# Kernel tuning notes

Measured on AMD Instinct MI355X. Metric: run time of the kernel, lower is better.

The kernel has to match this reference:

```python
import jax, jax.numpy as jnp
import numpy as np

# Module config (matches init_kwargs)
DIM = 256
NUM_HEADS = 8
AREA = 4
B, C, H, W = 8, DIM, 64, 64
HEAD_DIM = DIM // NUM_HEADS

# Each Conv in the source is Conv2d(bias=False) + BatchNorm2d + Identity (activation=False).
# In eval mode BN is a per-channel affine, so we represent each Conv as (weight, scale, bias).

def setup_inputs() -> dict:
    key = jax.random.key(0)
    ks = jax.random.split(key, 13)
    def w(k, shape, s=0.05):
        return jax.random.normal(k, shape, jnp.float32) * s
    def bn_scale(k, n):
        return 1.0 + 0.02 * jax.random.normal(k, (n,), jnp.float32)
    x = jax.random.normal(ks[0], (B, C, H, W), jnp.float32)
    return {
        "x": x,
        "w_qk": w(ks[1], (2 * C, C)),        # 1x1 conv: [out,in]
        "s_qk": bn_scale(ks[2], 2 * C),
        "b_qk": w(ks[3], (2 * C,), 0.01),
        "w_v": w(ks[4], (C, C)),
        "s_v": bn_scale(ks[5], C),
        "b_v": w(ks[6], (C,), 0.01),
        "w_pe": w(ks[7], (C, 1, 5, 5)),       # depthwise 5x5, groups=C
        "s_pe": bn_scale(ks[8], C),
        "b_pe": w(ks[9], (C,), 0.01),
        "w_proj": w(ks[10], (C, C)),
        "s_proj": bn_scale(ks[11], C),
        "b_proj": w(ks[12], (C,), 0.01),
    }


def _affine(y, s, b):
    # per-channel BN-eval affine on NCHW
    return y * s[None, :, None, None] + b[None, :, None, None]


def _conv1x1(x, w, s, b):
    return _affine(jnp.einsum('bchw,oc->bohw', x, w), s, b)


def reference(x, w_qk, s_qk, b_qk, w_v, s_v, b_v, w_pe, s_pe, b_pe, w_proj, s_proj, b_proj):
    N = H * W
    Na = N // AREA
    Ba = B * AREA

    qk = _conv1x1(x, w_qk, s_qk, b_qk)                    # [B, 2C, H, W]
    v4 = _conv1x1(x, w_v, s_v, b_v)                       # [B, C, H, W]
    pp = _affine(
        jax.lax.conv_general_dilated(
            v4, w_pe, (1, 1), 'SAME', feature_group_count=C,
            dimension_numbers=('NCHW', 'OIHW', 'NCHW')),
        s_pe, b_pe)                                        # [B, C, H, W]

    # flatten(2).transpose(1,2) then area split along N
    qk = qk.reshape(B, 2 * C, N).transpose(0, 2, 1).reshape(Ba, Na, 2 * C)
    v = v4.reshape(B, C, N).transpose(0, 2, 1).reshape(Ba, Na, C)

    q = qk[..., :C].reshape(Ba, Na, NUM_HEADS, HEAD_DIM)
    k = qk[..., C:].reshape(Ba, Na, NUM_HEADS, HEAD_DIM)
    vh = v.reshape(Ba, Na, NUM_HEADS, HEAD_DIM)

    scale = jnp.asarray(HEAD_DIM, jnp.float32) ** -0.5
    attn = jnp.einsum('bqhd,bkhd->bhqk', q, k) * scale     # [Ba, h, Na, Na]
    attn = jax.nn.softmax(attn, axis=-1)                   # max-stable softmax over keys
    o = jnp.einsum('bhqk,bkhd->bqhd', attn, vh)            # [Ba, Na, h, d]
    o = o.reshape(Ba, Na, C).reshape(B, N, C)
    o = o.reshape(B, H, W, C).transpose(0, 3, 1, 2)        # [B, C, H, W]

    return _conv1x1(o + pp, w_proj, s_proj, b_proj)
```

## Files before the change

### kernel.cpp

```cpp
#include <hip/hip_runtime.h>
#include <math.h>


#define NN 4096
#define NA 1024

typedef unsigned short us;
typedef __attribute__((ext_vector_type(4))) unsigned short us4;
typedef __attribute__((ext_vector_type(8))) unsigned short us8;
typedef __attribute__((ext_vector_type(8))) short bf16x8;
typedef __attribute__((ext_vector_type(4))) float f32x4;

#define QS (0.17677669529663687f * 1.4426950408889634f)

__device__ __forceinline__ us f2b(float f) {
    unsigned u = __builtin_bit_cast(unsigned, f);
    u += 0x7fffu + ((u >> 16) & 1u);
    return (us)(u >> 16);
}
__device__ __forceinline__ float b2f(us h) {
    unsigned u = ((unsigned)h) << 16;
    return __builtin_bit_cast(float, u);
}
__device__ __forceinline__ unsigned pack2(float lo, float hi) {
    return (unsigned)f2b(lo) | ((unsigned)f2b(hi) << 16);
}
__device__ __forceinline__ unsigned cvtpk_bf16(float lo, float hi) {
    unsigned r;
    asm("v_cvt_pk_bf16_f32 %0, %1, %2" : "=v"(r) : "v"(lo), "v"(hi));
    return r;
}
__device__ __forceinline__ float fexp2(float x) {
    float r;
    asm("v_exp_f32 %0, %1" : "=v"(r) : "v"(x));
    return r;
}

__device__ __forceinline__ size_t wswz(int ch, int k) {
    return ((size_t)((ch >> 4) * 8 + (k >> 5))) * 512 + ((((k >> 3) & 3) * 16 + (ch & 15))) * 8 + (k & 7);
}

__global__ __launch_bounds__(256) void prep_kernel(
    const float* __restrict__ w_qk, const float* __restrict__ s_qk, const float* __restrict__ b_qk,
    const float* __restrict__ w_v,  const float* __restrict__ s_v,
    const float* __restrict__ w_proj, const float* __restrict__ s_proj,
    us* __restrict__ wqkh, us* __restrict__ wvh, us* __restrict__ wprojh,
    float* __restrict__ bqkp)
{
    int idx = blockIdx.x * 256 + threadIdx.x;
    if (idx < 131072) {
        int o = idx >> 8, k = idx & 255;
        float sc = s_qk[o] * (o < 256 ? QS : 1.0f);
        wqkh[wswz(o, k)] = f2b(w_qk[idx] * sc);
    } else if (idx < 196608) {
        int j = idx - 131072; int o = j >> 8, k = j & 255;
        wvh[wswz(o, k)] = f2b(w_v[j] * s_v[o]);
    } else {
        int j = idx - 196608; int o = j >> 8, k = j & 255;
        wprojh[wswz(o, k)] = f2b(w_proj[j] * s_proj[o]);
    }
    if (idx < 512) bqkp[idx] = b_qk[idx] * (idx < 256 ? QS : 1.0f);
}

__global__ __launch_bounds__(256) void qkv_kernel(
    const float* __restrict__ x,
    const us* __restrict__ wqkh, const float* __restrict__ bqkp,
    const us* __restrict__ wvh,  const float* __restrict__ b_v,
    us* __restrict__ qt, us* __restrict__ vbuf)
{
    const int n0 = blockIdx.x * 64;
    const int b  = blockIdx.y;
    const int tid = threadIdx.x;
    const int w = tid >> 6, lane = tid & 63, c = lane & 15, g = lane >> 4;

    __shared__ __align__(16) us Xs[64][264];

    const float* Xb = x + (size_t)b * 256 * NN;
    #pragma unroll
    for (int i = 0; i < 16; i++) {
        int t = tid + i * 256;
        int cp = t >> 5, pp = t & 31;
        const float* r0 = Xb + (size_t)(2 * cp) * NN + n0 + 2 * pp;
        float2 a0 = *(const float2*)r0;
        float2 a1 = *(const float2*)(r0 + NN);
        *(unsigned*)&Xs[2 * pp][2 * cp]     = pack2(a0.x, a1.x);
        *(unsigned*)&Xs[2 * pp + 1][2 * cp] = pack2(a0.y, a1.y);
    }
    __syncthreads();

    for (int grp = 0; grp < 3; grp++) {
        f32x4 acc[4][4] = {};
        for (int kc = 0; kc < 256; kc += 32) {
            bf16x8 Xf[4];
            #pragma unroll
            for (int j = 0; j < 4; j++)
                Xf[j] = *(const bf16x8*)&Xs[j * 16 + c][kc + g * 8];
            #pragma unroll
            for (int cgi = 0; cgi < 4; cgi++) {
                int chbase = (grp < 2 ? (grp * 4 + cgi) * 64 : cgi * 64);
                const us* Wp = (grp < 2 ? wqkh : wvh) +
                    ((size_t)(((chbase >> 4) + w) * 8 + (kc >> 5))) * 512 + lane * 8;
                bf16x8 Wf = *(const bf16x8*)Wp;
                if (grp < 2) {
                    #pragma unroll
                    for (int j = 0; j < 4; j++)
                        acc[cgi][j] = __builtin_amdgcn_mfma_f32_16x16x32_bf16(Xf[j], Wf, acc[cgi][j], 0, 0, 0);
                } else {
                    #pragma unroll
                    for (int j = 0; j < 4; j++)
                        acc[cgi][j] = __builtin_amdgcn_mfma_f32_16x16x32_bf16(Wf, Xf[j], acc[cgi][j], 0, 0, 0);
                }
            }
        }
        if (grp < 2) {
            #pragma unroll
            for (int cgi = 0; cgi < 4; cgi++) {
                int ch = (grp * 4 + cgi) * 64 + w * 16 + c;
                float bb = bqkp[ch];
                #pragma unroll
                for (int j = 0; j < 4; j++)
                    #pragma unroll
                    for (int r = 0; r < 4; r++)
                        qt[((size_t)b * 4096 + n0 + j * 16 + g * 4 + r) * 512 + ch] =
                            f2b(acc[cgi][j][r] + bb);
            }
        } else {
            #pragma unroll
            for (int cgi = 0; cgi < 4; cgi++)
                #pragma unroll
                for (int r = 0; r < 4; r++) {
                    int ch = cgi * 64 + w * 16 + g * 4 + r;
                    float bb = b_v[ch];
                    #pragma unroll
                    for (int j = 0; j < 4; j++)
                        vbuf[((size_t)b * 256 + ch) * NN + n0 + j * 16 + c] =
                            f2b(acc[cgi][j][r] + bb);
                }
        }
    }
}

__global__ __launch_bounds__(256) void pe_conv_kernel(
    const us* __restrict__ vbuf,
    const float* __restrict__ w_pe, const float* __restrict__ s_pe, const float* __restrict__ b_pe,
    float* __restrict__ opp)
{
    const int c = blockIdx.x, b = blockIdx.y;
    const int tid = threadIdx.x;
    const us* vp = vbuf + ((size_t)b * 256 + c) * NN;
    __shared__ float plane[4096];
    __shared__ float wloc[25];
    #pragma unroll
    for (int i = 0; i < 4; i++) {
        int idx = tid + i * 256;
        us4 v = *(const us4*)&vp[idx * 4];
        float4 f;
        f.x = b2f(v[0]); f.y = b2f(v[1]); f.z = b2f(v[2]); f.w = b2f(v[3]);
        *(float4*)&plane[idx * 4] = f;
    }
    if (tid < 25) wloc[tid] = w_pe[c * 25 + tid];
    __syncthreads();

    const float s = s_pe[c], bb = b_pe[c];
    float* op = opp + ((size_t)b * 256 + c) * NN;
    for (int i = 0; i < 16; i++) {
        int pix = tid + i * 256;
        int ph = pix >> 6, pw = pix & 63;
        float acc = 0.f;
        #pragma unroll
        for (int dy = -2; dy <= 2; dy++) {
            int hy = ph + dy;
            if (hy < 0 || hy > 63) continue;
            #pragma unroll
            for (int dx = -2; dx <= 2; dx++) {
                int wx = pw + dx;
                if (wx < 0 || wx > 63) continue;
                acc += plane[hy * 64 + wx] * wloc[(dy + 2) * 5 + (dx + 2)];
            }
        }
        op[pix] = acc * s + bb;
    }
}

__global__ __launch_bounds__(256) void attn_kernel(
    const us* __restrict__ qt, const us* __restrict__ vbuf, float* __restrict__ opp)
{
    const int qtb = blockIdx.x;
    const int h   = blockIdx.y;
    const int ba  = blockIdx.z;
    const int b = ba >> 2, a = ba & 3;
    const int tid = threadIdx.x;
    const int w = tid >> 6, lane = tid & 63, c = lane & 15, g = lane >> 4;
    const int q0 = qtb * 128;

    __shared__ __align__(16) us Qt[128][40];
    __shared__ __align__(16) us Kt[2][64][40];
    __shared__ __align__(16) us Vs[2][2048];
    __shared__ __align__(16) us Ps[128][72];

    const int krow = tid >> 2, kseg = tid & 3;
    const int vrow = tid >> 3, vseg = tid & 7;
    const int vbyte = vrow * 128 + ((vseg ^ (vrow & 7)) << 4);

    const us* Kg = qt + ((size_t)b * 4096 + a * NA) * 512 + 256 + h * 32;
    const us* Vg = vbuf + ((size_t)b * 256 + h * 32) * NN + a * NA;

    #pragma unroll
    for (int i = 0; i < 2; i++) {
        int t = tid + i * 256;
        int row = t >> 2, seg = t & 3;
        *(us8*)&Qt[row][seg * 8] =
            *(const us8*)&qt[((size_t)b * 4096 + a * NA + q0 + row) * 512 + h * 32 + seg * 8];
    }
    {
        us8 kreg = *(const us8*)(Kg + (size_t)krow * 512 + kseg * 8);
        us8 vreg = *(const us8*)(Vg + (size_t)vrow * NN + vseg * 8);
        *(us8*)&Kt[0][krow][kseg * 8] = kreg;
        *(us8*)((char*)Vs[0] + vbyte) = vreg;
    }
    __syncthreads();

    const bf16x8 Qf0 = *(const bf16x8*)&Qt[w * 16 + c][g * 8];
    const bf16x8 Qf1 = *(const bf16x8*)&Qt[64 + w * 16 + c][g * 8];
    const bf16x8 ones = {0x3F80, 0x3F80, 0x3F80, 0x3F80, 0x3F80, 0x3F80, 0x3F80, 0x3F80};
    const f32x4 z = {0.f, 0.f, 0.f, 0.f};
    const int qr0 = w * 16 + c, qr1 = 64 + w * 16 + c;

    f32x4 O0a = z, O1a = z, Osa = z;
    f32x4 O0b = z, O1b = z, Osb = z;
    int cur = 0;

    for (int kt = 0; kt < 16; kt++) {
        us8 kreg, vreg;
        if (kt < 15) {
            const int kv1 = (kt + 1) * 64;
            kreg = *(const us8*)(Kg + ((size_t)(kv1 + krow)) * 512 + kseg * 8);
            vreg = *(const us8*)(Vg + (size_t)vrow * NN + kv1 + vseg * 8);
        }

        f32x4 sA[4], sB[4];
        #pragma unroll
        for (int j = 0; j < 4; j++) {
            bf16x8 Kf = *(const bf16x8*)&Kt[cur][j * 16 + c][g * 8];
            sA[j] = __builtin_amdgcn_mfma_f32_16x16x32_bf16(Kf, Qf0, z, 0, 0, 0);
            sB[j] = __builtin_amdgcn_mfma_f32_16x16x32_bf16(Kf, Qf1, z, 0, 0, 0);
        }

        #pragma unroll
        for (int j = 0; j < 4; j++) {
            uint2 pr;
            pr.x = cvtpk_bf16(fexp2(sA[j][0]), fexp2(sA[j][1]));
            pr.y = cvtpk_bf16(fexp2(sA[j][2]), fexp2(sA[j][3]));
            *(uint2*)&Ps[qr0][j * 16 + g * 4] = pr;
            uint2 qr_;
            qr_.x = cvtpk_bf16(fexp2(sB[j][0]), fexp2(sB[j][1]));
            qr_.y = cvtpk_bf16(fexp2(sB[j][2]), fexp2(sB[j][3]));
            *(uint2*)&Ps[qr1][j * 16 + g * 4] = qr_;
        }

        asm volatile("s_waitcnt lgkmcnt(0)" ::: "memory");
        __builtin_amdgcn_sched_barrier(0);

        #pragma unroll
        for (int ks = 0; ks < 2; ks++) {
            int so = (((ks * 4 + g) ^ (c & 7)) << 4);
            bf16x8 Bv0 = *(const bf16x8*)((char*)Vs[cur] + c * 128 + so);
            bf16x8 Bv1 = *(const bf16x8*)((char*)Vs[cur] + (16 + c) * 128 + so);
            bf16x8 Ap0 = *(const bf16x8*)&Ps[qr0][ks * 32 + g * 8];
            bf16x8 Ap1 = *(const bf16x8*)&Ps[qr1][ks * 32 + g * 8];
            O0a = __builtin_amdgcn_mfma_f32_16x16x32_bf16(Ap0, Bv0, O0a, 0, 0, 0);
            O1a = __builtin_amdgcn_mfma_f32_16x16x32_bf16(Ap0, Bv1, O1a, 0, 0, 0);
            Osa = __builtin_amdgcn_mfma_f32_16x16x32_bf16(Ap0, ones, Osa, 0, 0, 0);
            O0b = __builtin_amdgcn_mfma_f32_16x16x32_bf16(Ap1, Bv0, O0b, 0, 0, 0);
            O1b = __builtin_amdgcn_mfma_f32_16x16x32_bf16(Ap1, Bv1, O1b, 0, 0, 0);
            Osb = __builtin_amdgcn_mfma_f32_16x16x32_bf16(Ap1, ones, Osb, 0, 0, 0);
        }

        if (kt < 15) {
            *(us8*)&Kt[cur ^ 1][krow][kseg * 8] = kreg;
            *(us8*)((char*)Vs[cur ^ 1] + vbyte) = vreg;
        }
        __syncthreads();
        cur ^= 1;
    }

    float linva[4], linvb[4];
    #pragma unroll
    for (int r = 0; r < 4; r++) { linva[r] = 1.0f / Osa[r]; linvb[r] = 1.0f / Osb[r]; }

    float* Ob = opp + ((size_t)(b * 256 + h * 32)) * NN + a * NA + q0 + w * 16 + g * 4;
    {
        float4 o = *(float4*)(Ob + (size_t)c * NN);
        o.x += O0a[0] * linva[0]; o.y += O0a[1] * linva[1];
        o.z += O0a[2] * linva[2]; o.w += O0a[3] * linva[3];
        *(float4*)(Ob + (size_t)c * NN) = o;
        float4 o2 = *(float4*)(Ob + (size_t)(16 + c) * NN);
        o2.x += O1a[0] * linva[0]; o2.y += O1a[1] * linva[1];
        o2.z += O1a[2] * linva[2]; o2.w += O1a[3] * linva[3];
        *(float4*)(Ob + (size_t)(16 + c) * NN) = o2;

        float* Ob2 = Ob + 64;
        float4 o3 = *(float4*)(Ob2 + (size_t)c * NN);
        o3.x += O0b[0] * linvb[0]; o3.y += O0b[1] * linvb[1];
        o3.z += O0b[2] * linvb[2]; o3.w += O0b[3] * linvb[3];
        *(float4*)(Ob2 + (size_t)c * NN) = o3;
        float4 o4 = *(float4*)(Ob2 + (size_t)(16 + c) * NN);
        o4.x += O1b[0] * linvb[0]; o4.y += O1b[1] * linvb[1];
        o4.z += O1b[2] * linvb[2]; o4.w += O1b[3] * linvb[3];
        *(float4*)(Ob2 + (size_t)(16 + c) * NN) = o4;
    }
}

__global__ __launch_bounds__(256) void proj_kernel(
    const float* __restrict__ opp,
    const us* __restrict__ wprojh, const float* __restrict__ b_proj,
    float* __restrict__ out)
{
    const int n0 = blockIdx.x * 64;
    const int b  = blockIdx.y;
    const int tid = threadIdx.x;
    const int w = tid >> 6, lane = tid & 63, c = lane & 15, g = lane >> 4;

    __shared__ __align__(16) us Xs[64][264];

    const float* Xb = opp + (size_t)b * 256 * NN;
    #pragma unroll
    for (int i = 0; i < 16; i++) {
        int t = tid + i * 256;
        int cp = t >> 5, pp = t & 31;
        const float* r0 = Xb + (size_t)(2 * cp) * NN + n0 + 2 * pp;
        float2 a0 = *(const float2*)r0;
        float2 a1 = *(const float2*)(r0 + NN);
        *(unsigned*)&Xs[2 * pp][2 * cp]     = pack2(a0.x, a1.x);
        *(unsigned*)&Xs[2 * pp + 1][2 * cp] = pack2(a0.y, a1.y);
    }
    __syncthreads();

    f32x4 acc[4][4] = {};
    for (int kc = 0; kc < 256; kc += 32) {
        bf16x8 Xf[4];
        #pragma unroll
        for (int j = 0; j < 4; j++)
            Xf[j] = *(const bf16x8*)&Xs[j * 16 + c][kc + g * 8];
        #pragma unroll
        for (int cgi = 0; cgi < 4; cgi++) {
            const us* Wp = wprojh +
                ((size_t)((cgi * 4 + w) * 8 + (kc >> 5))) * 512 + lane * 8;
            bf16x8 Wf = *(const bf16x8*)Wp;
            #pragma unroll
            for (int j = 0; j < 4; j++)
                acc[cgi][j] = __builtin_amdgcn_mfma_f32_16x16x32_bf16(Wf, Xf[j], acc[cgi][j], 0, 0, 0);
        }
    }

    #pragma unroll
    for (int cgi = 0; cgi < 4; cgi++)
        #pragma unroll
        for (int r = 0; r < 4; r++) {
            int ch = cgi * 64 + w * 16 + g * 4 + r;
            float bb = b_proj[ch];
            #pragma unroll
            for (int j = 0; j < 4; j++)
                out[((size_t)b * 256 + ch) * NN + n0 + j * 16 + c] = acc[cgi][j][r] + bb;
        }
}

extern "C" void kernel_launch(void* const* d_in, const int* in_sizes, int n_in,
                              void* d_out, int out_size, void* d_ws, size_t ws_size,
                              hipStream_t stream) {
    const float* x      = (const float*)d_in[0];
    const float* w_qk   = (const float*)d_in[1];
    const float* s_qk   = (const float*)d_in[2];
    const float* b_qk   = (const float*)d_in[3];
    const float* w_v    = (const float*)d_in[4];
    const float* s_v    = (const float*)d_in[5];
    const float* b_v    = (const float*)d_in[6];
    const float* w_pe   = (const float*)d_in[7];
    const float* s_pe   = (const float*)d_in[8];
    const float* b_pe   = (const float*)d_in[9];
    const float* w_proj = (const float*)d_in[10];
    const float* s_proj = (const float*)d_in[11];
    const float* b_proj = (const float*)d_in[12];
    float* out = (float*)d_out;

    char* p = (char*)d_ws;
    us* qtb     = (us*)p;                  p += (size_t)8 * 4096 * 512 * 2;
    us* vbuf    = (us*)p;                  p += (size_t)8 * 256 * 4096 * 2;
    float* opp  = (float*)p;               p += (size_t)8 * 256 * 4096 * 4;
    us* wqkh    = (us*)p;                  p += (size_t)512 * 256 * 2;
    us* wvh     = (us*)p;                  p += (size_t)256 * 256 * 2;
    us* wprojh  = (us*)p;                  p += (size_t)256 * 256 * 2;
    float* bqkp = (float*)p;

    prep_kernel<<<1024, 256, 0, stream>>>(w_qk, s_qk, b_qk, w_v, s_v,
                                          w_proj, s_proj, wqkh, wvh, wprojh, bqkp);
    qkv_kernel<<<dim3(64, 8), 256, 0, stream>>>(x, wqkh, bqkp, wvh, b_v, qtb, vbuf);
    pe_conv_kernel<<<dim3(256, 8), 256, 0, stream>>>(vbuf, w_pe, s_pe, b_pe, opp);
    attn_kernel<<<dim3(8, 8, 32), 256, 0, stream>>>(qtb, vbuf, opp);
    proj_kernel<<<dim3(64, 8), 256, 0, stream>>>(opp, wprojh, b_proj, out);
}
```

Before: 156.7 us.

## Split softmax-PV into two halves to overlap exp with MFMA, load Q directly

The attention kernel now processes the second 64-query half's exp/convert after the first half's PV MFMAs are issued, so that exp work for half B overlaps MFMA execution for half A. It also drops the shared-memory Q staging tile and loads Q fragments straight from global memory into registers, and swaps the grid axes so heads map to blockIdx.x. The trade-off is an extra lgkmcnt wait and duplicated V fragment reads from LDS, plus higher register pressure from holding the packed half-B probabilities.

```diff
diff --git a/kernel.cpp b/kernel.cpp
--- a/kernel.cpp
+++ b/kernel.cpp
@@ -185,15 +185,14 @@
 __global__ __launch_bounds__(256) void attn_kernel(
     const us* __restrict__ qt, const us* __restrict__ vbuf, float* __restrict__ opp)
 {
-    const int qtb = blockIdx.x;
-    const int h   = blockIdx.y;
+    const int h   = blockIdx.x;
+    const int qtb = blockIdx.y;
     const int ba  = blockIdx.z;
     const int b = ba >> 2, a = ba & 3;
     const int tid = threadIdx.x;
     const int w = tid >> 6, lane = tid & 63, c = lane & 15, g = lane >> 4;
     const int q0 = qtb * 128;
 
-    __shared__ __align__(16) us Qt[128][40];
     __shared__ __align__(16) us Kt[2][64][40];
     __shared__ __align__(16) us Vs[2][2048];
     __shared__ __align__(16) us Ps[128][72];
@@ -205,13 +204,10 @@
     const us* Kg = qt + ((size_t)b * 4096 + a * NA) * 512 + 256 + h * 32;
     const us* Vg = vbuf + ((size_t)b * 256 + h * 32) * NN + a * NA;
 
-    #pragma unroll
-    for (int i = 0; i < 2; i++) {
-        int t = tid + i * 256;
-        int row = t >> 2, seg = t & 3;
-        *(us8*)&Qt[row][seg * 8] =
-            *(const us8*)&qt[((size_t)b * 4096 + a * NA + q0 + row) * 512 + h * 32 + seg * 8];
-    }
+    const us* Qp = qt + ((size_t)b * 4096 + a * NA + q0 + w * 16 + c) * 512 + h * 32 + g * 8;
+    const bf16x8 Qf0 = *(const bf16x8*)Qp;
+    const bf16x8 Qf1 = *(const bf16x8*)(Qp + (size_t)64 * 512);
+
     {
         us8 kreg = *(const us8*)(Kg + (size_t)krow * 512 + kseg * 8);
         us8 vreg = *(const us8*)(Vg + (size_t)vrow * NN + vseg * 8);
@@ -220,8 +216,6 @@
     }
     __syncthreads();
 
-    const bf16x8 Qf0 = *(const bf16x8*)&Qt[w * 16 + c][g * 8];
-    const bf16x8 Qf1 = *(const bf16x8*)&Qt[64 + w * 16 + c][g * 8];
     const bf16x8 ones = {0x3F80, 0x3F80, 0x3F80, 0x3F80, 0x3F80, 0x3F80, 0x3F80, 0x3F80};
     const f32x4 z = {0.f, 0.f, 0.f, 0.f};
     const int qr0 = w * 16 + c, qr1 = 64 + w * 16 + c;
@@ -252,14 +246,16 @@
             pr.x = cvtpk_bf16(fexp2(sA[j][0]), fexp2(sA[j][1]));
             pr.y = cvtpk_bf16(fexp2(sA[j][2]), fexp2(sA[j][3]));
             *(uint2*)&Ps[qr0][j * 16 + g * 4] = pr;
-            uint2 qr_;
-            qr_.x = cvtpk_bf16(fexp2(sB[j][0]), fexp2(sB[j][1]));
-            qr_.y = cvtpk_bf16(fexp2(sB[j][2]), fexp2(sB[j][3]));
-            *(uint2*)&Ps[qr1][j * 16 + g * 4] = qr_;
-        }
-
+        }
         asm volatile("s_waitcnt lgkmcnt(0)" ::: "memory");
         __builtin_amdgcn_sched_barrier(0);
+
+        uint2 prb[4];
+        #pragma unroll
+        for (int j = 0; j < 4; j++) {
+            prb[j].x = cvtpk_bf16(fexp2(sB[j][0]), fexp2(sB[j][1]));
+            prb[j].y = cvtpk_bf16(fexp2(sB[j][2]), fexp2(sB[j][3]));
+        }
 
         #pragma unroll
         for (int ks = 0; ks < 2; ks++) {
@@ -267,10 +263,23 @@
             bf16x8 Bv0 = *(const bf16x8*)((char*)Vs[cur] + c * 128 + so);
             bf16x8 Bv1 = *(const bf16x8*)((char*)Vs[cur] + (16 + c) * 128 + so);
             bf16x8 Ap0 = *(const bf16x8*)&Ps[qr0][ks * 32 + g * 8];
-            bf16x8 Ap1 = *(const bf16x8*)&Ps[qr1][ks * 32 + g * 8];
             O0a = __builtin_amdgcn_mfma_f32_16x16x32_bf16(Ap0, Bv0, O0a, 0, 0, 0);
             O1a = __builtin_amdgcn_mfma_f32_16x16x32_bf16(Ap0, Bv1, O1a, 0, 0, 0);
             Osa = __builtin_amdgcn_mfma_f32_16x16x32_bf16(Ap0, ones, Osa, 0, 0, 0);
+        }
+
+        #pragma unroll
+        for (int j = 0; j < 4; j++)
+            *(uint2*)&Ps[qr1][j * 16 + g * 4] = prb[j];
+        asm volatile("s_waitcnt lgkmcnt(0)" ::: "memory");
+        __builtin_amdgcn_sched_barrier(0);
+
+        #pragma unroll
+        for (int ks = 0; ks < 2; ks++) {
+            int so = (((ks * 4 + g) ^ (c & 7)) << 4);
+            bf16x8 Bv0 = *(const bf16x8*)((char*)Vs[cur] + c * 128 + so);
+            bf16x8 Bv1 = *(const bf16x8*)((char*)Vs[cur] + (16 + c) * 128 + so);
+            bf16x8 Ap1 = *(const bf16x8*)&Ps[qr1][ks * 32 + g * 8];
             O0b = __builtin_amdgcn_mfma_f32_16x16x32_bf16(Ap1, Bv0, O0b, 0, 0, 0);
             O1b = __builtin_amdgcn_mfma_f32_16x16x32_bf16(Ap1, Bv1, O1b, 0, 0, 0);
             Osb = __builtin_amdgcn_mfma_f32_16x16x32_bf16(Ap1, ones, Osb, 0, 0, 0);
```

Measured after the change: 155.8 us. About the same (-0.6%).
